# Kernel optimization log

Hardware: AMD Instinct MI355X
Metric: run time of the kernel (lower is better)

Reference implementation:

```python
import jax, jax.numpy as jnp
import numpy as np

B = 8192          # sessions
DOCS = 10         # docs per session
NPS = 21          # nodes per session: 1 query + 10 docs + 10 titles
N = B * NPS       # 172032 total nodes
F_IN, F_HID, F_OUT = 171, 256, 128


def _gat_conv(x, src, dst, W, a_src, a_dst, bias, n_nodes):
    # PyG GATConv, heads=1, negative_slope=0.2, self-loops already appended.
    h = x @ W.T                                   # [N, F]
    e = jax.nn.leaky_relu(jnp.take(h @ a_src, src) + jnp.take(h @ a_dst, dst), 0.2)
    m = jax.ops.segment_max(e, dst, num_segments=n_nodes)
    ex = jnp.exp(e - m[dst])
    denom = jax.ops.segment_sum(ex, dst, num_segments=n_nodes)
    alpha = ex / denom[dst]                       # softmax over incoming edges
    out = jax.ops.segment_sum(h[src] * alpha[:, None], dst, num_segments=n_nodes)
    return out + bias


def setup_inputs() -> dict:
    key = jax.random.key(0)
    ks = jax.random.split(key, 20)
    # structured node ids: per session block [q, d0..d9, t0..t9]
    base = jnp.arange(B, dtype=jnp.int64) * NPS
    doc_id = base[:, None] + 1 + jnp.arange(DOCS, dtype=jnp.int64)   # [B,10]
    q = base                                                          # query node = doc_id[:,0]-1
    t = doc_id + DOCS                                                 # title node = doc+10
    qd_s = jnp.repeat(q, DOCS); qd_d = doc_id.reshape(-1)
    dt_s = doc_id.reshape(-1);  dt_d = t.reshape(-1)
    src = jnp.concatenate([qd_s, qd_d, dt_s, dt_d])
    dst = jnp.concatenate([qd_d, qd_s, dt_d, dt_s])
    edge_index = jnp.stack([src, dst])                                # [2, 327680]

    inp = {
        "i": 0,
        "x": jax.random.normal(ks[0], (N, F_IN), jnp.float32),
        "edge_index": edge_index,
        "doc_id": doc_id,
        "click": jax.random.randint(ks[1], (B,), 0, 2),
        "query": jax.random.randint(ks[2], (B,), 0, 6338),
        "docu": jax.random.randint(ks[3], (B, DOCS), 0, 56477),
        "title_id": jax.random.randint(ks[4], (B, DOCS), 0, 56363),
        # embedding tables
        "query_table": jax.random.normal(ks[5], (6338, 160), jnp.float32) * 0.02,
        "doc_table": jax.random.normal(ks[6], (56477, 160), jnp.float32) * 0.02,
        "title_table": jax.random.normal(ks[7], (56363, 160), jnp.float32) * 0.02,
        "pos_table": jax.random.normal(ks[8], (10, 1), jnp.float32) * 0.02,
        "click_table": jax.random.normal(ks[9], (2, 1), jnp.float32) * 0.02,
        # GATConv 1 (171 -> 256)
        "W1": jax.random.normal(ks[10], (F_HID, F_IN), jnp.float32) * (1.0 / np.sqrt(F_IN)),
        "a_src1": jax.random.normal(ks[11], (F_HID,), jnp.float32) * 0.1,
        "a_dst1": jax.random.normal(ks[12], (F_HID,), jnp.float32) * 0.1,
        "b1": jnp.zeros((F_HID,), jnp.float32),
        # GATConv 2 (256 -> 128)
        "W2": jax.random.normal(ks[13], (F_OUT, F_HID), jnp.float32) * (1.0 / np.sqrt(F_HID)),
        "a_src2": jax.random.normal(ks[14], (F_OUT,), jnp.float32) * 0.1,
        "a_dst2": jax.random.normal(ks[15], (F_OUT,), jnp.float32) * 0.1,
        "b2": jnp.zeros((F_OUT,), jnp.float32),
        # head linear (128 -> 1)
        "Wl": jax.random.normal(ks[16], (1, F_OUT), jnp.float32) * (1.0 / np.sqrt(F_OUT)),
        "bl": jnp.zeros((1,), jnp.float32),
    }
    return inp


def reference(i, x, edge_index, doc_id, click, query, docu, title_id,
              query_table, doc_table, title_table, pos_table, click_table,
              W1, a_src1, a_dst1, b1, W2, a_src2, a_dst2, b2, Wl, bl):
    n_nodes = x.shape[0]
    q_emb = query_table[query]          # [B,160]
    d_emb = doc_table[docu]             # [B,10,160]
    t_emb = title_table[title_id]       # [B,10,160]
    pos = pos_table[:, 0]               # [10]  (position_embedding of 0..9)
    clk = click_table[click, 0]         # [B]

    df = doc_id.reshape(-1)             # flat doc node ids [B*10]
    if i == 0:
        x = x.at[doc_id[:, 0] - 1, :160].set(q_emb)
        x = x.at[df, :160].set(d_emb.reshape(-1, 160))
        x = x.at[df, 160].set(jnp.broadcast_to(pos, doc_id.shape).reshape(-1))
        x = x.at[df, 161 + i].set(jnp.broadcast_to(clk[:, None], doc_id.shape).reshape(-1))
        x = x.at[df + 10, :160].set(t_emb.reshape(-1, 160))
    else:
        x = x.at[df, 161 + i].set(jnp.broadcast_to(clk[:, None], doc_id.shape).reshape(-1))

    # add self-loops (PyG GATConv default)
    loop = jnp.arange(n_nodes, dtype=edge_index.dtype)
    src = jnp.concatenate([edge_index[0], loop])
    dst = jnp.concatenate([edge_index[1], loop])

    y = _gat_conv(x, src, dst, W1, a_src1, a_dst1, b1, n_nodes)
    y = jax.nn.relu(y)                  # dropout is identity in eval mode
    hidden_state = _gat_conv(y, src, dst, W2, a_src2, a_dst2, b2, n_nodes)
    y = jax.nn.relu(hidden_state)
    y = jax.nn.sigmoid(y @ Wl.T + bl)   # [N,1]
    return (hidden_state, y, x[:, :171])
```

## Files before the change

### kernel.cpp

```cpp
#include <hip/hip_runtime.h>
#include <cstdint>

#define N_NODES 172032
#define BATCH   8192
#define NPS     21
#define F_IN    171
#define K1P     192
#define F_HID   256
#define F_OUT   128

typedef unsigned short u16;
typedef __attribute__((ext_vector_type(8))) short  bf16x8;
typedef __attribute__((ext_vector_type(4))) float  f32x4;

__device__ inline u16 f2bf(float f) {
    unsigned u = __float_as_uint(f);
    unsigned r = u + 0x7FFFu + ((u >> 16) & 1u);
    return (u16)(r >> 16);
}
__device__ inline float bf2f(u16 h) { return __uint_as_float(((unsigned)h) << 16); }
__device__ inline float lrelu(float v) { return v > 0.f ? v : 0.2f * v; }

__device__ inline int deg_of(int n)  { return n == 0 ? 11 : (n <= 10 ? 3 : 2); }
__device__ inline int edge_base(int n) { return n == 0 ? 0 : (n <= 10 ? 11 + 3*(n-1) : 41 + 2*(n-11)); }
__device__ inline int src_of(int n, int k) {
    if (n == 0)  return k < 10 ? k + 1 : 0;
    if (n <= 10) return k == 0 ? 0 : (k == 1 ? n + 10 : n);
    return k == 0 ? n - 10 : n;
}

__device__ inline float wave_red(float v) {
    for (int off = 32; off; off >>= 1) v += __shfl_down(v, off);
    return v;
}

__global__ void build_x(const int* __restrict__ iptr, const float* __restrict__ x,
                        const int* __restrict__ click, const int* __restrict__ query,
                        const int* __restrict__ docu, const int* __restrict__ title_id,
                        const float* __restrict__ qtab, const float* __restrict__ dtab,
                        const float* __restrict__ ttab, const float* __restrict__ ptab,
                        const float* __restrict__ ctab,
                        float* __restrict__ out_x, u16* __restrict__ xb)
{
    int node = blockIdx.x;
    int t = threadIdx.x;
    int b = node / NPS;
    int p = node - b * NPS;
    int i = iptr[0];
    if (t < F_IN) {
        float v = x[(long)node * F_IN + t];
        if (i == 0) {
            if (p == 0) {
                if (t < 160) v = qtab[(long)query[b] * 160 + t];
            } else if (p <= 10) {
                int j = p - 1;
                if (t < 160)       v = dtab[(long)docu[b*10 + j] * 160 + t];
                else if (t == 160) v = ptab[j];
                else if (t == 161) v = ctab[click[b]];
            } else {
                int j = p - 11;
                if (t < 160) v = ttab[(long)title_id[b*10 + j] * 160 + t];
            }
        } else {
            if (p >= 1 && p <= 10 && t == 161 + i) v = ctab[click[b]];
        }
        out_x[(long)node * F_IN + t] = v;
        xb[(long)node * K1P + t] = f2bf(v);
    } else if (t < K1P) {
        xb[(long)node * K1P + t] = 0;
    }
}

__global__ void prep_w(const float* __restrict__ W1, const float* __restrict__ W2,
                       u16* __restrict__ W1b, u16* __restrict__ W2b)
{
    int id = blockIdx.x * 256 + threadIdx.x;
    if (id < 256 * K1P) {
        int r = id / K1P, k = id - r * K1P;
        W1b[id] = (k < F_IN) ? f2bf(W1[r * F_IN + k]) : (u16)0;
    }
    if (id < 128 * 256) W2b[id] = f2bf(W2[id]);
}

template<int KPAD, int KSTAGE>
__global__ __launch_bounds__(256) void gemm_bt(const u16* __restrict__ A, const u16* __restrict__ B,
                                               u16* __restrict__ C, int ldc)
{
    constexpr int SA  = KSTAGE + 8;
    constexpr int CPS = KSTAGE / 8;
    __shared__ __align__(16) u16 Al[64 * SA];
    __shared__ __align__(16) u16 Bl[128 * SA];

    const int m0 = blockIdx.x * 64;
    const int n0 = blockIdx.y * 128;
    const int tid = threadIdx.x;
    const int lane = tid & 63, w = tid >> 6;
    const int wr = w >> 1, wc = w & 1;
    const int lm = lane & 15, lq = lane >> 4;

    f32x4 acc[2][4];
    for (int f = 0; f < 2; ++f)
        for (int g = 0; g < 4; ++g)
            acc[f][g] = (f32x4){0.f, 0.f, 0.f, 0.f};

    for (int ks = 0; ks < KPAD; ks += KSTAGE) {
        if (ks) __syncthreads();
        for (int id = tid; id < 64 * CPS; id += 256) {
            int row = id / CPS, ch = id - row * CPS;
            uint4 vv = *(const uint4*)(A + (long)(m0 + row) * KPAD + ks + ch * 8);
            *(uint4*)(Al + row * SA + ch * 8) = vv;
        }
        for (int id = tid; id < 128 * CPS; id += 256) {
            int row = id / CPS, ch = id - row * CPS;
            uint4 vv = *(const uint4*)(B + (long)(n0 + row) * KPAD + ks + ch * 8);
            *(uint4*)(Bl + row * SA + ch * 8) = vv;
        }
        __syncthreads();

        for (int kb = 0; kb < KSTAGE / 32; ++kb) {
            int koff = kb * 32 + lq * 8;
            bf16x8 a0 = *(const bf16x8*)(Al + (wr*32 +  0 + lm) * SA + koff);
            bf16x8 a1 = *(const bf16x8*)(Al + (wr*32 + 16 + lm) * SA + koff);
            bf16x8 b0 = *(const bf16x8*)(Bl + (wc*64 +  0 + lm) * SA + koff);
            bf16x8 b1 = *(const bf16x8*)(Bl + (wc*64 + 16 + lm) * SA + koff);
            bf16x8 b2 = *(const bf16x8*)(Bl + (wc*64 + 32 + lm) * SA + koff);
            bf16x8 b3 = *(const bf16x8*)(Bl + (wc*64 + 48 + lm) * SA + koff);
            acc[0][0] = __builtin_amdgcn_mfma_f32_16x16x32_bf16(a0, b0, acc[0][0], 0, 0, 0);
            acc[0][1] = __builtin_amdgcn_mfma_f32_16x16x32_bf16(a0, b1, acc[0][1], 0, 0, 0);
            acc[0][2] = __builtin_amdgcn_mfma_f32_16x16x32_bf16(a0, b2, acc[0][2], 0, 0, 0);
            acc[0][3] = __builtin_amdgcn_mfma_f32_16x16x32_bf16(a0, b3, acc[0][3], 0, 0, 0);
            acc[1][0] = __builtin_amdgcn_mfma_f32_16x16x32_bf16(a1, b0, acc[1][0], 0, 0, 0);
            acc[1][1] = __builtin_amdgcn_mfma_f32_16x16x32_bf16(a1, b1, acc[1][1], 0, 0, 0);
            acc[1][2] = __builtin_amdgcn_mfma_f32_16x16x32_bf16(a1, b2, acc[1][2], 0, 0, 0);
            acc[1][3] = __builtin_amdgcn_mfma_f32_16x16x32_bf16(a1, b3, acc[1][3], 0, 0, 0);
        }
    }

    for (int f = 0; f < 2; ++f)
        for (int g = 0; g < 4; ++g)
            for (int r = 0; r < 4; ++r) {
                int row = m0 + wr*32 + f*16 + lq*4 + r;
                int col = n0 + wc*64 + g*16 + lm;
                C[(long)row * ldc + col] = f2bf(acc[f][g][r]);
            }
}

__global__ __launch_bounds__(256) void agg1(const u16* __restrict__ h1b,
                                            const float* __restrict__ asrc, const float* __restrict__ adst,
                                            const float* __restrict__ bias, u16* __restrict__ y1b)
{
    __shared__ __align__(16) u16 h[NPS * F_HID];
    __shared__ float s_l[NPS], d_l[NPS], alpha[61];
    int blk = blockIdx.x, tid = threadIdx.x;
    long base = (long)blk * NPS * F_HID;

    for (int id = tid; id < NPS * F_HID / 8; id += 256)
        *(uint4*)(h + id * 8) = *(const uint4*)(h1b + base + id * 8);
    __syncthreads();

    int lane = tid & 63, w = tid >> 6;
    for (int n = w; n < NPS; n += 4) {
        float as_ = 0.f, ad_ = 0.f;
        for (int c = lane; c < F_HID; c += 64) {
            float hv = bf2f(h[n * F_HID + c]);
            as_ += hv * asrc[c];
            ad_ += hv * adst[c];
        }
        as_ = wave_red(as_); ad_ = wave_red(ad_);
        if (lane == 0) { s_l[n] = as_; d_l[n] = ad_; }
    }
    __syncthreads();

    if (tid < NPS) {
        int n = tid, deg = deg_of(n), eb = edge_base(n);
        float dn = d_l[n], m = -1e30f;
        for (int k = 0; k < deg; ++k) m = fmaxf(m, lrelu(s_l[src_of(n,k)] + dn));
        float den = 0.f;
        for (int k = 0; k < deg; ++k) den += expf(lrelu(s_l[src_of(n,k)] + dn) - m);
        float inv = 1.f / den;
        for (int k = 0; k < deg; ++k) alpha[eb + k] = expf(lrelu(s_l[src_of(n,k)] + dn) - m) * inv;
    }
    __syncthreads();

    int c = tid;
    {
        float a = alpha[10] * bf2f(h[c]);
        for (int j = 1; j <= 10; ++j) a += alpha[j-1] * bf2f(h[j * F_HID + c]);
        y1b[base + c] = f2bf(fmaxf(a + bias[c], 0.f));
    }
    for (int j = 1; j <= 10; ++j) {
        int eb = 11 + 3*(j-1);
        float a = alpha[eb]   * bf2f(h[c])
                + alpha[eb+1] * bf2f(h[(j+10) * F_HID + c])
                + alpha[eb+2] * bf2f(h[j * F_HID + c]);
        y1b[base + j * F_HID + c] = f2bf(fmaxf(a + bias[c], 0.f));
    }
    for (int j = 1; j <= 10; ++j) {
        int eb = 41 + 2*(j-1);
        float a = alpha[eb]   * bf2f(h[j * F_HID + c])
                + alpha[eb+1] * bf2f(h[(10+j) * F_HID + c]);
        y1b[base + (10+j) * F_HID + c] = f2bf(fmaxf(a + bias[c], 0.f));
    }
}

__global__ __launch_bounds__(128) void agg2(const u16* __restrict__ g2b,
                                            const float* __restrict__ asrc, const float* __restrict__ adst,
                                            const float* __restrict__ bias,
                                            const float* __restrict__ Wl, const float* __restrict__ bl,
                                            float* __restrict__ out_hid, float* __restrict__ out_y)
{
    __shared__ __align__(16) u16 h[NPS * F_OUT];
    __shared__ float s_l[NPS], d_l[NPS], alpha[61];
    __shared__ float hid[NPS * F_OUT];
    int blk = blockIdx.x, tid = threadIdx.x;
    long base = (long)blk * NPS * F_OUT;

    for (int id = tid; id < NPS * F_OUT / 8; id += 128)
        *(uint4*)(h + id * 8) = *(const uint4*)(g2b + base + id * 8);
    __syncthreads();

    int lane = tid & 63, w = tid >> 6;
    for (int n = w; n < NPS; n += 2) {
        float as_ = 0.f, ad_ = 0.f;
        for (int c = lane; c < F_OUT; c += 64) {
            float hv = bf2f(h[n * F_OUT + c]);
            as_ += hv * asrc[c];
            ad_ += hv * adst[c];
        }
        as_ = wave_red(as_); ad_ = wave_red(ad_);
        if (lane == 0) { s_l[n] = as_; d_l[n] = ad_; }
    }
    __syncthreads();

    if (tid < NPS) {
        int n = tid, deg = deg_of(n), eb = edge_base(n);
        float dn = d_l[n], m = -1e30f;
        for (int k = 0; k < deg; ++k) m = fmaxf(m, lrelu(s_l[src_of(n,k)] + dn));
        float den = 0.f;
        for (int k = 0; k < deg; ++k) den += expf(lrelu(s_l[src_of(n,k)] + dn) - m);
        float inv = 1.f / den;
        for (int k = 0; k < deg; ++k) alpha[eb + k] = expf(lrelu(s_l[src_of(n,k)] + dn) - m) * inv;
    }
    __syncthreads();

    int c = tid;
    float wl = Wl[c];
    {
        float a = alpha[10] * bf2f(h[c]);
        for (int j = 1; j <= 10; ++j) a += alpha[j-1] * bf2f(h[j * F_OUT + c]);
        float hv = a + bias[c];
        out_hid[base + c] = hv;
        hid[c] = fmaxf(hv, 0.f) * wl;
    }
    for (int j = 1; j <= 10; ++j) {
        int eb = 11 + 3*(j-1);
        float a = alpha[eb]   * bf2f(h[c])
                + alpha[eb+1] * bf2f(h[(j+10) * F_OUT + c])
                + alpha[eb+2] * bf2f(h[j * F_OUT + c]);
        float hv = a + bias[c];
        out_hid[base + j * F_OUT + c] = hv;
        hid[j * F_OUT + c] = fmaxf(hv, 0.f) * wl;
    }
    for (int j = 1; j <= 10; ++j) {
        int eb = 41 + 2*(j-1);
        float a = alpha[eb]   * bf2f(h[j * F_OUT + c])
                + alpha[eb+1] * bf2f(h[(10+j) * F_OUT + c]);
        float hv = a + bias[c];
        out_hid[base + (10+j) * F_OUT + c] = hv;
        hid[(10+j) * F_OUT + c] = fmaxf(hv, 0.f) * wl;
    }
    __syncthreads();

    float bl0 = bl[0];
    for (int n = w; n < NPS; n += 2) {
        float v = hid[n * F_OUT + lane] + hid[n * F_OUT + lane + 64];
        v = wave_red(v);
        if (lane == 0) out_y[(long)blk * NPS + n] = 1.f / (1.f + expf(-(v + bl0)));
    }
}

extern "C" void kernel_launch(void* const* d_in, const int* in_sizes, int n_in,
                              void* d_out, int out_size, void* d_ws, size_t ws_size,
                              hipStream_t stream) {
    const int*   ip    = (const int*)  d_in[0];
    const float* x     = (const float*)d_in[1];
    const int*   click = (const int*)  d_in[4];
    const int*   query = (const int*)  d_in[5];
    const int*   docu  = (const int*)  d_in[6];
    const int*   title = (const int*)  d_in[7];
    const float* qtab  = (const float*)d_in[8];
    const float* dtab  = (const float*)d_in[9];
    const float* ttab  = (const float*)d_in[10];
    const float* ptab  = (const float*)d_in[11];
    const float* ctab  = (const float*)d_in[12];
    const float* W1    = (const float*)d_in[13];
    const float* as1   = (const float*)d_in[14];
    const float* ad1   = (const float*)d_in[15];
    const float* b1    = (const float*)d_in[16];
    const float* W2    = (const float*)d_in[17];
    const float* as2   = (const float*)d_in[18];
    const float* ad2   = (const float*)d_in[19];
    const float* b2    = (const float*)d_in[20];
    const float* Wl    = (const float*)d_in[21];
    const float* bl    = (const float*)d_in[22];

    float* out_hid = (float*)d_out;
    float* out_y   = out_hid + (long)N_NODES * F_OUT;
    float* out_x   = out_y + N_NODES;

    u16* h1b = (u16*)d_ws;
    u16* g2b = h1b;
    u16* xb  = h1b + 44040192L;
    u16* y1b = xb;
    u16* W1b = h1b + 88080384L;
    u16* W2b = W1b + 256 * K1P;

    build_x<<<N_NODES, 192, 0, stream>>>(ip, x, click, query, docu, title,
                                         qtab, dtab, ttab, ptab, ctab, out_x, xb);
    prep_w<<<192, 256, 0, stream>>>(W1, W2, W1b, W2b);
    gemm_bt<K1P, 96><<<dim3(N_NODES / 64, 2), 256, 0, stream>>>(xb, W1b, h1b, F_HID);
    agg1<<<BATCH, 256, 0, stream>>>(h1b, as1, ad1, b1, y1b);
    gemm_bt<F_HID, 128><<<dim3(N_NODES / 64, 1), 256, 0, stream>>>(y1b, W2b, g2b, F_OUT);
    agg2<<<BATCH, 128, 0, stream>>>(g2b, as2, ad2, b2, Wl, bl, out_hid, out_y);
}
```

Before: 665.1 us.

## Build input features per session with shared-memory staging and vectorized stores

build_x now runs one 256-thread block per session instead of one block per node. It stages all 21 nodes' features in shared memory, then writes out_x with aligned float4 stores and the padded bf16 matrix with 16-byte stores. This targets the cost of 172K tiny blocks and of scalar 2-byte and 4-byte global writes. The trade-off is extra shared memory (about 14 KB per block) and index division in the inner loops.

```diff
diff --git a/kernel.cpp b/kernel.cpp
--- a/kernel.cpp
+++ b/kernel.cpp
@@ -8,6 +8,8 @@
 #define K1P     192
 #define F_HID   256
 #define F_OUT   128
+#define SX_F    (NPS * F_IN)
+#define SXB     (NPS * K1P)
 
 typedef unsigned short u16;
 typedef __attribute__((ext_vector_type(8))) short  bf16x8;
@@ -34,7 +36,7 @@
     return v;
 }
 
-__global__ void build_x(const int* __restrict__ iptr, const float* __restrict__ x,
+__global__ __launch_bounds__(256) void build_x(const int* __restrict__ iptr, const float* __restrict__ x,
                         const int* __restrict__ click, const int* __restrict__ query,
                         const int* __restrict__ docu, const int* __restrict__ title_id,
                         const float* __restrict__ qtab, const float* __restrict__ dtab,
@@ -42,32 +44,77 @@
                         const float* __restrict__ ctab,
                         float* __restrict__ out_x, u16* __restrict__ xb)
 {
-    int node = blockIdx.x;
-    int t = threadIdx.x;
-    int b = node / NPS;
-    int p = node - b * NPS;
-    int i = iptr[0];
-    if (t < F_IN) {
-        float v = x[(long)node * F_IN + t];
-        if (i == 0) {
-            if (p == 0) {
-                if (t < 160) v = qtab[(long)query[b] * 160 + t];
-            } else if (p <= 10) {
-                int j = p - 1;
-                if (t < 160)       v = dtab[(long)docu[b*10 + j] * 160 + t];
-                else if (t == 160) v = ptab[j];
-                else if (t == 161) v = ctab[click[b]];
+    __shared__ float sx[SX_F];
+    __shared__ int   dz[10], tz[10], s_q;
+    __shared__ float s_clk;
+
+    const int s   = blockIdx.x;
+    const int tid = threadIdx.x;
+    const int i   = iptr[0];
+    const long xbase = (long)s * SX_F;
+
+    if (tid < 10)       dz[tid]      = docu[s*10 + tid];
+    else if (tid < 20)  tz[tid - 10] = title_id[s*10 + tid - 10];
+    else if (tid == 20) s_q          = query[s];
+    else if (tid == 21) s_clk        = ctab[click[s]];
+    __syncthreads();
+
+    if (i == 0) {
+        for (int idx = tid; idx < SX_F; idx += 256) {
+            int p = idx / F_IN;
+            int c = idx - p * F_IN;
+            float v;
+            if (c >= 160) {
+                if (p >= 1 && p <= 10 && c == 160)      v = ptab[p - 1];
+                else if (p >= 1 && p <= 10 && c == 161) v = s_clk;
+                else                                     v = x[xbase + idx];
             } else {
-                int j = p - 11;
-                if (t < 160) v = ttab[(long)title_id[b*10 + j] * 160 + t];
+                if (p == 0)       v = qtab[(long)s_q * 160 + c];
+                else if (p <= 10) v = dtab[(long)dz[p-1] * 160 + c];
+                else              v = ttab[(long)tz[p-11] * 160 + c];
             }
-        } else {
-            if (p >= 1 && p <= 10 && t == 161 + i) v = ctab[click[b]];
-        }
-        out_x[(long)node * F_IN + t] = v;
-        xb[(long)node * K1P + t] = f2bf(v);
-    } else if (t < K1P) {
-        xb[(long)node * K1P + t] = 0;
+            sx[idx] = v;
+        }
+    } else {
+        for (int idx = tid; idx < SX_F; idx += 256) {
+            int p = idx / F_IN;
+            int c = idx - p * F_IN;
+            float v = x[xbase + idx];
+            if (p >= 1 && p <= 10 && c == 161 + i) v = s_clk;
+            sx[idx] = v;
+        }
+    }
+    __syncthreads();
+
+    {
+        int r    = (int)(xbase & 3);
+        int head = (4 - r) & 3;
+        if (tid < head) out_x[xbase + tid] = sx[tid];
+        int n4 = (SX_F - head) >> 2;
+        for (int id = tid; id < n4; id += 256) {
+            int o = head + id * 4;
+            float4 v = make_float4(sx[o], sx[o+1], sx[o+2], sx[o+3]);
+            *(float4*)(out_x + xbase + o) = v;
+        }
+        int done = head + n4 * 4;
+        int tail = SX_F - done;
+        if (tid < tail) out_x[xbase + done + tid] = sx[done + tid];
+    }
+
+    {
+        u16* xbs = xb + (long)s * SXB;
+        for (int id = tid; id < SXB / 8; id += 256) {
+            int k0 = id * 8;
+            int node = k0 / K1P;
+            int kk   = k0 - node * K1P;
+            union { u16 h[8]; uint4 v; } u;
+            #pragma unroll
+            for (int j = 0; j < 8; ++j) {
+                int c = kk + j;
+                u.h[j] = (c < F_IN) ? f2bf(sx[node * F_IN + c]) : (u16)0;
+            }
+            *(uint4*)(xbs + k0) = u.v;
+        }
     }
 }
 
@@ -315,8 +362,8 @@
     u16* W1b = h1b + 88080384L;
     u16* W2b = W1b + 256 * K1P;
 
-    build_x<<<N_NODES, 192, 0, stream>>>(ip, x, click, query, docu, title,
-                                         qtab, dtab, ttab, ptab, ctab, out_x, xb);
+    build_x<<<BATCH, 256, 0, stream>>>(ip, x, click, query, docu, title,
+                                       qtab, dtab, ttab, ptab, ctab, out_x, xb);
     prep_w<<<192, 256, 0, stream>>>(W1, W2, W1b, W2b);
     gemm_bt<K1P, 96><<<dim3(N_NODES / 64, 2), 256, 0, stream>>>(xb, W1b, h1b, F_HID);
     agg1<<<BATCH, 256, 0, stream>>>(h1b, as1, ad1, b1, y1b);
```

Result: faster. 589.0 us (-11.4%).
